# Kernel optimization log

Measured on AMD Instinct MI355X. Metric: run time of the kernel, lower is better.

Reference implementation:

```python
import jax, jax.numpy as jnp
import numpy as np

# dims: L=tgt len, S=src len, N=batch, E=embed, H=heads
L, S, N, E, H = 1024, 1024, 4, 1024, 16
HD = E // H  # head dim = 64


def setup_inputs() -> dict:
    key = jax.random.key(0)
    ks = jax.random.split(key, 7)
    w_scale = 0.02
    return {
        "query": jax.random.normal(ks[0], (L, N, E), jnp.float32),
        "key": jax.random.normal(ks[1], (S, N, E), jnp.float32),
        "value": jax.random.normal(ks[2], (S, N, E), jnp.float32),
        "in_proj_weight": jax.random.normal(ks[3], (3 * E, E), jnp.float32) * w_scale,
        "in_proj_bias": jax.random.normal(ks[4], (3 * E,), jnp.float32) * w_scale,
        "out_proj_weight": jax.random.normal(ks[5], (E, E), jnp.float32) * w_scale,
        "out_proj_bias": jax.random.normal(ks[6], (E,), jnp.float32) * w_scale,
    }


def reference(query, key, value, in_proj_weight, in_proj_bias,
              out_proj_weight, out_proj_bias):
    scaling = float(HD) ** -0.5
    # packed QKV projection, sliced exactly as the torch code does
    q = (query @ in_proj_weight[:E].T + in_proj_bias[:E]) * scaling        # (L,N,E)
    k = key @ in_proj_weight[E:2 * E].T + in_proj_bias[E:2 * E]            # (S,N,E)
    v = value @ in_proj_weight[2 * E:].T + in_proj_bias[2 * E:]            # (S,N,E)
    # split heads: (L,N,E) -> (N*H, L, HD)
    q = q.reshape(L, N * H, HD).transpose(1, 0, 2)
    k = k.reshape(S, N * H, HD).transpose(1, 0, 2)
    v = v.reshape(S, N * H, HD).transpose(1, 0, 2)
    scores = jnp.einsum('bld,bsd->bls', q, k)          # (N*H, L, S)
    attn = jax.nn.softmax(scores, axis=-1)
    sig = jax.nn.sigmoid(scores)                        # the need_sigmoid_weights variant
    out = jnp.einsum('bls,bsd->bld', attn, v)          # (N*H, L, HD)
    out = out.transpose(1, 0, 2).reshape(L, N, E)
    out = out @ out_proj_weight.T + out_proj_bias       # (L,N,E)
    # weights averaged over heads, as torch MHA returns: (N,L,S)
    attn_weights = attn.reshape(N, H, L, S).sum(axis=1) / H
    sig_weights = sig.reshape(N, H, L, S).sum(axis=1) / H
    return out, attn_weights, sig_weights
```

## Files before the change

kernel.cpp:

```cpp
#include <hip/hip_runtime.h>

#define L_DIM 1024
#define E_DIM 1024
#define NB 4
#define H_NUM 16
#define HD_DIM 64
#define T_TOK 4096
#define NHB 64

typedef float f32x4 __attribute__((ext_vector_type(4)));
typedef unsigned short u16x8 __attribute__((ext_vector_type(8)));
typedef unsigned short u16x4 __attribute__((ext_vector_type(4)));
typedef __bf16 bf16x8 __attribute__((ext_vector_type(8)));

__device__ inline unsigned short f2bf(float f) {
  unsigned int u = __builtin_bit_cast(unsigned int, f);
  u += 0x7FFFu + ((u >> 16) & 1u);
  return (unsigned short)(u >> 16);
}
__device__ inline f32x4 mfma16(u16x8 a, u16x8 b, f32x4 c) {
  return __builtin_amdgcn_mfma_f32_16x16x32_bf16(
      __builtin_bit_cast(bf16x8, a), __builtin_bit_cast(bf16x8, b), c, 0, 0, 0);
}

__device__ __forceinline__ void gl2lds16(const void* g, void* l) {
  auto gp = reinterpret_cast<const __attribute__((address_space(1))) unsigned int*>(
      reinterpret_cast<unsigned long long>(g));
  auto lp = reinterpret_cast<__attribute__((address_space(3))) unsigned int*>(
      static_cast<unsigned int>(reinterpret_cast<unsigned long long>(l)));
  __builtin_amdgcn_global_load_lds(gp, lp, 16, 0, 0);
}

__global__ __launch_bounds__(256) void cast_kernel(
    const float* __restrict__ s0, const float* __restrict__ s1,
    const float* __restrict__ s2, const float* __restrict__ s3,
    unsigned short* __restrict__ d0, unsigned short* __restrict__ d1,
    unsigned short* __restrict__ d2, unsigned short* __restrict__ d3,
    int n0, int n1, int n2, int n3) {
  const int y = blockIdx.y;
  const float* s = (y == 0) ? s0 : (y == 1) ? s1 : (y == 2) ? s2 : s3;
  unsigned short* d = (y == 0) ? d0 : (y == 1) ? d1 : (y == 2) ? d2 : d3;
  const int n = (y == 0) ? n0 : (y == 1) ? n1 : (y == 2) ? n2 : n3;
  int idx = (blockIdx.x * 256 + threadIdx.x) * 8;
  const int stride = gridDim.x * 256 * 8;
  for (; idx < n; idx += stride) {
    float4 a = *(const float4*)(s + idx);
    float4 b = *(const float4*)(s + idx + 4);
    u16x8 o = {f2bf(a.x), f2bf(a.y), f2bf(a.z), f2bf(a.w),
               f2bf(b.x), f2bf(b.y), f2bf(b.z), f2bf(b.w)};
    *(u16x8*)(d + idx) = o;
  }
}

__device__ __forceinline__ void stage_tile(const unsigned short* __restrict__ g,
                                           unsigned short* lbuf, int tid) {
  const int r = tid >> 2, c = tid & 3;
  const int sc = c ^ ((r ^ (r >> 2)) & 3);
  gl2lds16(g + (size_t)r * 1024 + sc * 8, lbuf + tid * 8);
  const int r2 = r + 64;
  gl2lds16(g + (size_t)r2 * 1024 + sc * 8, lbuf + (tid + 256) * 8);
}
__device__ __forceinline__ int frag_off(int r, int q) {
  return r * 32 + ((q ^ ((r ^ (r >> 2)) & 3)) << 3);
}

__global__ __launch_bounds__(256) void qkv_gemm(
    const unsigned short* __restrict__ qb, const unsigned short* __restrict__ kb,
    const unsigned short* __restrict__ vb, const unsigned short* __restrict__ Wb,
    const float* __restrict__ bias, unsigned short* __restrict__ q_hm,
    unsigned short* __restrict__ k_hm, unsigned short* __restrict__ v_t) {
  __shared__ __align__(16) unsigned short As[2][4096];
  __shared__ __align__(16) unsigned short Bs[2][4096];
  const int tid = threadIdx.x;
  const int bm = blockIdx.x, bn = blockIdx.y, z = blockIdx.z;
  const unsigned short* Ag = ((z == 0) ? qb : (z == 1) ? kb : vb) + (size_t)bm * 128 * 1024;
  const unsigned short* Bg = Wb + (size_t)z * 1048576 + (size_t)bn * 128 * 1024;
  const float* bc = bias + z * E_DIM;

  const int w = tid >> 6, lane = tid & 63;
  const int wm = w & 1, wn = w >> 1;
  const int quad = lane >> 4, l16 = lane & 15;

  f32x4 acc[4][4];
#pragma unroll
  for (int i = 0; i < 4; i++)
#pragma unroll
    for (int j = 0; j < 4; j++) { f32x4 zz = {0.f, 0.f, 0.f, 0.f}; acc[i][j] = zz; }

  stage_tile(Ag, As[0], tid);
  stage_tile(Bg, Bs[0], tid);

  for (int kk = 0; kk < 32; kk++) {
    __syncthreads();
    if (kk + 1 < 32) {
      const int bf = (kk + 1) & 1;
      stage_tile(Ag + (kk + 1) * 32, As[bf], tid);
      stage_tile(Bg + (kk + 1) * 32, Bs[bf], tid);
    }
    const int cb = kk & 1;
    u16x8 af[4], bfv[4];
#pragma unroll
    for (int mi = 0; mi < 4; mi++) {
      int r = wm * 64 + mi * 16 + l16;
      af[mi] = *(const u16x8*)&As[cb][frag_off(r, quad)];
    }
#pragma unroll
    for (int ni = 0; ni < 4; ni++) {
      int r = wn * 64 + ni * 16 + l16;
      bfv[ni] = *(const u16x8*)&Bs[cb][frag_off(r, quad)];
    }
#pragma unroll
    for (int mi = 0; mi < 4; mi++)
#pragma unroll
      for (int ni = 0; ni < 4; ni++)
        acc[mi][ni] = mfma16(af[mi], bfv[ni], acc[mi][ni]);
  }
#pragma unroll
  for (int ni = 0; ni < 4; ni++) {
    int col = bn * 128 + wn * 64 + ni * 16 + l16;
    float bv = bc[col];
    int h = col >> 6, d = col & 63;
#pragma unroll
    for (int mi = 0; mi < 4; mi++) {
#pragma unroll
      for (int r = 0; r < 4; r++) {
        int t = bm * 128 + wm * 64 + mi * 16 + quad * 4 + r;
        float v = acc[mi][ni][r] + bv;
        int nb = t & 3, pos = t >> 2;
        if (z == 0) {
          v *= 0.125f;
          q_hm[(size_t)((nb * 16 + h) * 1024 + pos) * 64 + d] = f2bf(v);
        } else if (z == 1) {
          k_hm[(size_t)((nb * 16 + h) * 1024 + pos) * 64 + d] = f2bf(v);
        } else {
          v_t[(size_t)((nb * 16 + h) * 64 + d) * 1024 + pos] = f2bf(v);
        }
      }
    }
  }
}

__global__ __launch_bounds__(256, 2) void attn_kernel(
    const unsigned short* __restrict__ q_hm, const unsigned short* __restrict__ k_hm,
    const unsigned short* __restrict__ v_t, unsigned short* __restrict__ o_h,
    float* __restrict__ m_ws, float* __restrict__ r_ws) {
  __shared__ __align__(16) unsigned short stage[8][4096];
  __shared__ __align__(16) unsigned short pt[2][32][68];
  __shared__ float red_m[4][32];
  __shared__ float red_s[4][32];

  const int tid = threadIdx.x;
  const int flat = blockIdx.x + (blockIdx.y << 5);
  const int nf = (flat & 7) * 256 + (flat >> 3);
  const int l0 = (nf & 31) * 32;
  const int b = nf >> 5;
  const int nb = b >> 4, h = b & 15;
  const int w = tid >> 6, lane = tid & 63;
  const int quad = lane >> 4, l16 = lane & 15;

  const int i1 = tid + 256;
  const int r0s = tid >> 3, c0s = tid & 7;
  const int r1s = i1 >> 3, c1s = i1 & 7;
  const int src0 = (c0s ^ (r0s & 7)) * 8;
  const int src1 = (c1s ^ (r1s & 7)) * 8;

  const unsigned short* kbase = k_hm + ((size_t)b << 16);
  const unsigned short* vbase = v_t + ((size_t)b << 16);

  u16x8 bq[2][2];
#pragma unroll
  for (int g = 0; g < 2; g++) {
    const unsigned short* qp =
        q_hm + ((size_t)(b * 1024 + l0 + g * 16 + l16) << 6) + quad * 8;
    bq[g][0] = *(const u16x8*)qp;
    bq[g][1] = *(const u16x8*)(qp + 32);
  }
  asm volatile("" ::: "memory");

  f32x4 acc[16][2];
#pragma unroll
  for (int j = 0; j < 16; j++)
#pragma unroll
    for (int g = 0; g < 2; g++) { f32x4 z = {0.f, 0.f, 0.f, 0.f}; acc[j][g] = z; }

#pragma unroll
  for (int t = 0; t < 3; t++) {
    gl2lds16(kbase + ((size_t)(t * 64 + r0s) << 6) + src0, &stage[t][tid * 8]);
    gl2lds16(kbase + ((size_t)(t * 64 + r1s) << 6) + src1, &stage[t][i1 * 8]);
  }

  const int myrow = w * 16 + l16;
  const int sw0 = ((quad ^ (l16 & 7)) * 8);
  const int sw1 = (((quad + 4) ^ (l16 & 7)) * 8);

#pragma unroll
  for (int j = 0; j < 16; j++) {
    if (j + 3 < 16) {
      gl2lds16(kbase + ((size_t)((j + 3) * 64 + r0s) << 6) + src0,
               &stage[(j + 3) & 7][tid * 8]);
      gl2lds16(kbase + ((size_t)((j + 3) * 64 + r1s) << 6) + src1,
               &stage[(j + 3) & 7][i1 * 8]);
    } else {
      const int vt = j + 3 - 16;
      gl2lds16(vbase + ((size_t)r0s << 10) + vt * 64 + src0,
               &stage[(j + 3) & 7][tid * 8]);
      gl2lds16(vbase + ((size_t)r1s << 10) + vt * 64 + src1,
               &stage[(j + 3) & 7][i1 * 8]);
    }
    asm volatile("s_waitcnt vmcnt(6)" ::: "memory");
    __builtin_amdgcn_s_barrier();
    asm volatile("" ::: "memory");
    const unsigned short* kt = &stage[j & 7][myrow * 64];
    u16x8 ak0 = *(const u16x8*)(kt + sw0);
    u16x8 ak1 = *(const u16x8*)(kt + sw1);
    acc[j][0] = mfma16(ak0, bq[0][0], acc[j][0]);
    acc[j][0] = mfma16(ak1, bq[0][1], acc[j][0]);
    acc[j][1] = mfma16(ak0, bq[1][0], acc[j][1]);
    acc[j][1] = mfma16(ak1, bq[1][1], acc[j][1]);
  }

  float lm0 = -3e38f, lm1 = -3e38f;
#pragma unroll
  for (int j = 0; j < 16; j++)
#pragma unroll
    for (int r = 0; r < 4; r++) {
      lm0 = fmaxf(lm0, acc[j][0][r]);
      lm1 = fmaxf(lm1, acc[j][1][r]);
    }
  lm0 = fmaxf(lm0, __shfl_xor(lm0, 16, 64));
  lm0 = fmaxf(lm0, __shfl_xor(lm0, 32, 64));
  lm1 = fmaxf(lm1, __shfl_xor(lm1, 16, 64));
  lm1 = fmaxf(lm1, __shfl_xor(lm1, 32, 64));
  if (lane < 16) { red_m[w][lane] = lm0; red_m[w][lane + 16] = lm1; }
  asm volatile("s_waitcnt lgkmcnt(0)" ::: "memory");
  __builtin_amdgcn_s_barrier();
  asm volatile("" ::: "memory");
  float m0 = fmaxf(fmaxf(red_m[0][l16], red_m[1][l16]),
                   fmaxf(red_m[2][l16], red_m[3][l16]));
  float m1 = fmaxf(fmaxf(red_m[0][l16 + 16], red_m[1][l16 + 16]),
                   fmaxf(red_m[2][l16 + 16], red_m[3][l16 + 16]));
  float mm = 0.f;
  if (tid < 32)
    mm = fmaxf(fmaxf(red_m[0][tid], red_m[1][tid]),
               fmaxf(red_m[2][tid], red_m[3][tid]));

  float ls0 = 0.f, ls1 = 0.f;
#pragma unroll
  for (int j = 0; j < 16; j++) {
#pragma unroll
    for (int r = 0; r < 4; r++) {
      float e0 = __expf(acc[j][0][r] - m0);
      float e1 = __expf(acc[j][1][r] - m1);
      acc[j][0][r] = e0;
      acc[j][1][r] = e1;
      ls0 += e0;
      ls1 += e1;
    }
  }
  ls0 += __shfl_xor(ls0, 16, 64);
  ls0 += __shfl_xor(ls0, 32, 64);
  ls1 += __shfl_xor(ls1, 16, 64);
  ls1 += __shfl_xor(ls1, 32, 64);
  if (lane < 16) { red_s[w][lane] = ls0; red_s[w][lane + 16] = ls1; }
  asm volatile("s_waitcnt lgkmcnt(0)" ::: "memory");
  __builtin_amdgcn_s_barrier();
  asm volatile("" ::: "memory");
  float rv0 = 1.0f / (red_s[0][l16] + red_s[1][l16] + red_s[2][l16] + red_s[3][l16]);
  float rv1 = 1.0f / (red_s[0][l16 + 16] + red_s[1][l16 + 16] +
                      red_s[2][l16 + 16] + red_s[3][l16 + 16]);
  float ssv = 1.f;
  if (tid < 32)
    ssv = red_s[0][tid] + red_s[1][tid] + red_s[2][tid] + red_s[3][tid];

  {
    u16x4 p0 = {f2bf(acc[0][0][0]), f2bf(acc[0][0][1]), f2bf(acc[0][0][2]), f2bf(acc[0][0][3])};
    u16x4 p1 = {f2bf(acc[0][1][0]), f2bf(acc[0][1][1]), f2bf(acc[0][1][2]), f2bf(acc[0][1][3])};
    *(u16x4*)&pt[0][l16][w * 16 + quad * 4] = p0;
    *(u16x4*)&pt[0][16 + l16][w * 16 + quad * 4] = p1;
  }

  f32x4 oacc0 = {0.f, 0.f, 0.f, 0.f};
  f32x4 oacc1 = {0.f, 0.f, 0.f, 0.f};
#pragma unroll
  for (int j = 0; j < 16; j++) {
    if (j < 13) {
      const int t = j + 3;
      gl2lds16(vbase + ((size_t)r0s << 10) + t * 64 + src0, &stage[t & 7][tid * 8]);
      gl2lds16(vbase + ((size_t)r1s << 10) + t * 64 + src1, &stage[t & 7][i1 * 8]);
      asm volatile("s_waitcnt vmcnt(6) lgkmcnt(0)" ::: "memory");
    } else if (j == 13) {
      asm volatile("s_waitcnt vmcnt(4) lgkmcnt(0)" ::: "memory");
    } else if (j == 14) {
      asm volatile("s_waitcnt vmcnt(2) lgkmcnt(0)" ::: "memory");
    } else {
      asm volatile("s_waitcnt vmcnt(0) lgkmcnt(0)" ::: "memory");
    }
    __builtin_amdgcn_s_barrier();
    asm volatile("" ::: "memory");
    if (j < 15) {
      const int bf = (j + 1) & 1;
      u16x4 p0 = {f2bf(acc[j + 1][0][0]), f2bf(acc[j + 1][0][1]),
                  f2bf(acc[j + 1][0][2]), f2bf(acc[j + 1][0][3])};
      u16x4 p1 = {f2bf(acc[j + 1][1][0]), f2bf(acc[j + 1][1][1]),
                  f2bf(acc[j + 1][1][2]), f2bf(acc[j + 1][1][3])};
      *(u16x4*)&pt[bf][l16][w * 16 + quad * 4] = p0;
      *(u16x4*)&pt[bf][16 + l16][w * 16 + quad * 4] = p1;
    }
    const unsigned short* vt = &stage[j & 7][myrow * 64];
    u16x8 bv0 = *(const u16x8*)(vt + sw0);
    u16x8 bv1 = *(const u16x8*)(vt + sw1);
    u16x8 ap00 = *(const u16x8*)&pt[j & 1][l16][quad * 8];
    u16x8 ap01 = *(const u16x8*)&pt[j & 1][l16][32 + quad * 8];
    u16x8 ap10 = *(const u16x8*)&pt[j & 1][16 + l16][quad * 8];
    u16x8 ap11 = *(const u16x8*)&pt[j & 1][16 + l16][32 + quad * 8];
    oacc0 = mfma16(ap00, bv0, oacc0);
    oacc0 = mfma16(ap01, bv1, oacc0);
    oacc1 = mfma16(ap10, bv0, oacc1);
    oacc1 = mfma16(ap11, bv1, oacc1);
  }

  if (tid < 32) {
    m_ws[b * 1024 + l0 + tid] = mm;
    r_ws[b * 1024 + l0 + tid] = 1.0f / ssv;
  }

#pragma unroll
  for (int r = 0; r < 4; r++) {
    int lr = quad * 4 + r;
    float rr0 = __shfl(rv0, lr, 64);
    float rr1 = __shfl(rv1, lr, 64);
    int t0 = (l0 + lr) * 4 + nb;
    int t1 = (l0 + 16 + lr) * 4 + nb;
    o_h[((size_t)t0 << 10) + h * 64 + w * 16 + l16] = f2bf(oacc0[r] * rr0);
    o_h[((size_t)t1 << 10) + h * 64 + w * 16 + l16] = f2bf(oacc1[r] * rr1);
  }
}

__global__ __launch_bounds__(256, 2) void weights_kernel(
    const unsigned short* __restrict__ q_hm, const unsigned short* __restrict__ k_hm,
    const float* __restrict__ m_ws, const float* __restrict__ r_ws,
    float* __restrict__ attn_out, float* __restrict__ sig_out) {
  __shared__ __align__(16) unsigned short qs[4][4096];
  __shared__ __align__(16) unsigned short ks[4][4096];
  __shared__ float ml[16][64];
  __shared__ float rl[16][64];
  __shared__ float cl[16][64];

  const int tid = threadIdx.x;
  const int flat = blockIdx.x + (blockIdx.y << 4) + (blockIdx.z << 8);
  const int xcd = flat & 7, local = flat >> 3;
  const int nb = xcd >> 1;
  const int idx2 = ((xcd & 1) << 7) + local;
  const int l0 = (idx2 >> 4) << 6;
  const int s0 = (idx2 & 15) << 6;

  const int w = tid >> 6, lane = tid & 63;
  const int quad = lane >> 4, l16 = lane & 15;

  const int i1 = tid + 256;
  const int r0s = tid >> 3, c0s = tid & 7;
  const int r1s = i1 >> 3, c1s = i1 & 7;
  const int src0 = (c0s ^ (r0s & 7)) * 8;
  const int src1 = (c1s ^ (r1s & 7)) * 8;

  {
    int idx = tid * 4;
    int hh = idx >> 6, ii = idx & 63;
    int bb = nb * 16 + hh;
    float4 mv4 = *(const float4*)&m_ws[bb * 1024 + l0 + ii];
    float4 rv4 = *(const float4*)&r_ws[bb * 1024 + l0 + ii];
    *(float4*)&ml[hh][ii] = mv4;
    *(float4*)&rl[hh][ii] = rv4;
    float4 cv4 = {__expf(-mv4.x), __expf(-mv4.y), __expf(-mv4.z), __expf(-mv4.w)};
    *(float4*)&cl[hh][ii] = cv4;
  }

  const int sw0 = ((quad ^ (l16 & 7)) * 8);
  const int sw1 = (((quad + 4) ^ (l16 & 7)) * 8);

  auto stageQK = [&](int h) {
    const int bb = nb * 16 + h;
    const unsigned short* qb = q_hm + ((size_t)(bb * 1024 + l0) << 6);
    const unsigned short* kb = k_hm + ((size_t)(bb * 1024 + s0) << 6);
    const int bf = h & 3;
    gl2lds16(qb + (r0s << 6) + src0, &qs[bf][tid * 8]);
    gl2lds16(qb + (r1s << 6) + src1, &qs[bf][i1 * 8]);
    gl2lds16(kb + (r0s << 6) + src0, &ks[bf][tid * 8]);
    gl2lds16(kb + (r1s << 6) + src1, &ks[bf][i1 * 8]);
  };

  f32x4 accA[4], accS[4];
#pragma unroll
  for (int i = 0; i < 4; i++) {
    f32x4 zz = {0.f, 0.f, 0.f, 0.f};
    accA[i] = zz; accS[i] = zz;
  }

  stageQK(0);
  stageQK(1);
  asm volatile("s_waitcnt lgkmcnt(0)" ::: "memory");

  auto computeH = [&](int h) {
    const int bf = h & 3;
    const unsigned short* qt = &qs[bf][(w * 16 + l16) * 64];
    u16x8 a0 = *(const u16x8*)(qt + sw0);
    u16x8 a1 = *(const u16x8*)(qt + sw1);
    f32x4 mv = *(const f32x4*)&ml[h][w * 16 + quad * 4];
    f32x4 rv = *(const f32x4*)&rl[h][w * 16 + quad * 4];
    f32x4 cv = *(const f32x4*)&cl[h][w * 16 + quad * 4];
#pragma unroll
    for (int ni = 0; ni < 4; ni++) {
      const unsigned short* kt = &ks[bf][(ni * 16 + l16) * 64];
      u16x8 b0 = *(const u16x8*)(kt + sw0);
      u16x8 b1 = *(const u16x8*)(kt + sw1);
      f32x4 scv = {0.f, 0.f, 0.f, 0.f};
      scv = mfma16(a0, b0, scv);
      scv = mfma16(a1, b1, scv);
#pragma unroll
      for (int r = 0; r < 4; r++) {
        float e = __expf(scv[r] - mv[r]);
        accA[ni][r] += e * rv[r];
        accS[ni][r] += e * __builtin_amdgcn_rcpf(e + cv[r]);
      }
    }
  };

#pragma unroll 1
  for (int h = 0; h < 14; ++h) {
    stageQK(h + 2);
    asm volatile("s_waitcnt vmcnt(8)" ::: "memory");
    __builtin_amdgcn_s_barrier();
    asm volatile("" ::: "memory");
    computeH(h);
  }
  asm volatile("s_waitcnt vmcnt(4)" ::: "memory");
  __builtin_amdgcn_s_barrier();
  asm volatile("" ::: "memory");
  computeH(14);
  asm volatile("s_waitcnt vmcnt(0)" ::: "memory");
  __builtin_amdgcn_s_barrier();
  asm volatile("" ::: "memory");
  computeH(15);

  const float inv_h = 1.0f / 16.0f;
  const int lrow0 = l0 + w * 16;
#pragma unroll
  for (int ni = 0; ni < 4; ni++) {
#pragma unroll
    for (int r = 0; r < 4; r++) {
      int l = lrow0 + quad * 4 + r;
      int s = s0 + ni * 16 + l16;
      size_t idx = ((size_t)nb * 1024 + l) * 1024 + s;
      attn_out[idx] = accA[ni][r] * inv_h;
      sig_out[idx] = accS[ni][r] * inv_h;
    }
  }
}

__global__ __launch_bounds__(256) void out_gemm(
    const unsigned short* __restrict__ o_h, const unsigned short* __restrict__ Wb,
    const float* __restrict__ bias, float* __restrict__ out) {
  __shared__ __align__(16) unsigned short As[2][4096];
  __shared__ __align__(16) unsigned short Bs[2][4096];
  const int tid = threadIdx.x;
  const int bm = blockIdx.x, bn = blockIdx.y;
  const unsigned short* Ag = o_h + (size_t)bm * 128 * 1024;
  const unsigned short* Bg = Wb + (size_t)bn * 128 * 1024;

  const int w = tid >> 6, lane = tid & 63;
  const int wm = w & 1, wn = w >> 1;
  const int quad = lane >> 4, l16 = lane & 15;

  f32x4 acc[4][4];
#pragma unroll
  for (int i = 0; i < 4; i++)
#pragma unroll
    for (int j = 0; j < 4; j++) { f32x4 zz = {0.f, 0.f, 0.f, 0.f}; acc[i][j] = zz; }

  stage_tile(Ag, As[0], tid);
  stage_tile(Bg, Bs[0], tid);

  for (int kk = 0; kk < 32; kk++) {
    __syncthreads();
    if (kk + 1 < 32) {
      const int bf = (kk + 1) & 1;
      stage_tile(Ag + (kk + 1) * 32, As[bf], tid);
      stage_tile(Bg + (kk + 1) * 32, Bs[bf], tid);
    }
    const int cb = kk & 1;
    u16x8 af[4], bfv[4];
#pragma unroll
    for (int mi = 0; mi < 4; mi++) {
      int r = wm * 64 + mi * 16 + l16;
      af[mi] = *(const u16x8*)&As[cb][frag_off(r, quad)];
    }
#pragma unroll
    for (int ni = 0; ni < 4; ni++) {
      int r = wn * 64 + ni * 16 + l16;
      bfv[ni] = *(const u16x8*)&Bs[cb][frag_off(r, quad)];
    }
#pragma unroll
    for (int mi = 0; mi < 4; mi++)
#pragma unroll
      for (int ni = 0; ni < 4; ni++)
        acc[mi][ni] = mfma16(af[mi], bfv[ni], acc[mi][ni]);
  }
#pragma unroll
  for (int ni = 0; ni < 4; ni++) {
    int col = bn * 128 + wn * 64 + ni * 16 + l16;
    float bv = bias[col];
#pragma unroll
    for (int mi = 0; mi < 4; mi++) {
#pragma unroll
      for (int r = 0; r < 4; r++) {
        int t = bm * 128 + wm * 64 + mi * 16 + quad * 4 + r;
        out[(size_t)t * E_DIM + col] = acc[mi][ni][r] + bv;
      }
    }
  }
}

extern "C" void kernel_launch(void* const* d_in, const int* in_sizes, int n_in,
                              void* d_out, int out_size, void* d_ws, size_t ws_size,
                              hipStream_t stream) {
  const float* qin  = (const float*)d_in[0];
  const float* kin  = (const float*)d_in[1];
  const float* vin  = (const float*)d_in[2];
  const float* Wqkv = (const float*)d_in[3];
  const float* bqkv = (const float*)d_in[4];
  const float* Wout = (const float*)d_in[5];
  const float* bout = (const float*)d_in[6];
  float* out      = (float*)d_out;
  float* attn_out = out + 4194304;
  float* sig_out  = out + 8388608;

  unsigned short* q_hm = (unsigned short*)d_ws;
  unsigned short* k_hm = q_hm + 4194304;
  unsigned short* v_t  = q_hm + 8388608;
  unsigned short* o_h  = q_hm + 12582912;
  float* m_ws = (float*)(q_hm + 16777216);
  float* r_ws = m_ws + 65536;

  unsigned short* qb = (unsigned short*)(out + 4194304);
  unsigned short* kb = qb + 4194304;
  unsigned short* vb = qb + 8388608;
  unsigned short* Wqkvb = o_h;
  unsigned short* Woutb = v_t;

  cast_kernel<<<dim3(2048, 4), 256, 0, stream>>>(
      qin, kin, vin, Wqkv, qb, kb, vb, Wqkvb,
      4194304, 4194304, 4194304, 3145728);
  qkv_gemm<<<dim3(32, 8, 3), 256, 0, stream>>>(qb, kb, vb, Wqkvb, bqkv,
                                               q_hm, k_hm, v_t);
  attn_kernel<<<dim3(32, 64), 256, 0, stream>>>(q_hm, k_hm, v_t, o_h, m_ws, r_ws);
  cast_kernel<<<dim3(512, 1), 256, 0, stream>>>(
      Wout, Wout, Wout, Wout, Woutb, Woutb, Woutb, Woutb,
      1048576, 0, 0, 0);
  weights_kernel<<<dim3(16, 16, 4), 256, 0, stream>>>(q_hm, k_hm, m_ws, r_ws,
                                                      attn_out, sig_out);
  out_gemm<<<dim3(32, 8), 256, 0, stream>>>(o_h, Woutb, bout, out);
}
```

Measured before the change: 252.2 us.

## Deepen GEMM LDS pipeline to five stages and swizzle block order

New measurement: 266.4 us. 5.6% more time.

```diff
diff --git a/kernel.cpp b/kernel.cpp
--- a/kernel.cpp
+++ b/kernel.cpp
@@ -69,10 +69,12 @@
     const unsigned short* __restrict__ vb, const unsigned short* __restrict__ Wb,
     const float* __restrict__ bias, unsigned short* __restrict__ q_hm,
     unsigned short* __restrict__ k_hm, unsigned short* __restrict__ v_t) {
-  __shared__ __align__(16) unsigned short As[2][4096];
-  __shared__ __align__(16) unsigned short Bs[2][4096];
+  __shared__ __align__(16) unsigned short As[5][4096];
+  __shared__ __align__(16) unsigned short Bs[5][4096];
   const int tid = threadIdx.x;
-  const int bm = blockIdx.x, bn = blockIdx.y, z = blockIdx.z;
+  const int flat = blockIdx.x + (blockIdx.y << 5) + (blockIdx.z << 8);
+  const int nf = (flat & 7) * 96 + (flat >> 3);
+  const int bm = nf & 31, bn = (nf >> 5) & 7, z = nf >> 8;
   const unsigned short* Ag = ((z == 0) ? qb : (z == 1) ? kb : vb) + (size_t)bm * 128 * 1024;
   const unsigned short* Bg = Wb + (size_t)z * 1048576 + (size_t)bn * 128 * 1024;
   const float* bc = bias + z * E_DIM;
@@ -87,17 +89,29 @@
 #pragma unroll
     for (int j = 0; j < 4; j++) { f32x4 zz = {0.f, 0.f, 0.f, 0.f}; acc[i][j] = zz; }
 
-  stage_tile(Ag, As[0], tid);
-  stage_tile(Bg, Bs[0], tid);
-
+#pragma unroll
+  for (int t = 0; t < 3; t++) {
+    stage_tile(Ag + t * 32, As[t], tid);
+    stage_tile(Bg + t * 32, Bs[t], tid);
+  }
+
+  int cb = 0, sb = 3;
+#pragma unroll 1
   for (int kk = 0; kk < 32; kk++) {
-    __syncthreads();
-    if (kk + 1 < 32) {
-      const int bf = (kk + 1) & 1;
-      stage_tile(Ag + (kk + 1) * 32, As[bf], tid);
-      stage_tile(Bg + (kk + 1) * 32, Bs[bf], tid);
-    }
-    const int cb = kk & 1;
+    if (kk < 29) {
+      stage_tile(Ag + (kk + 3) * 32, As[sb], tid);
+      stage_tile(Bg + (kk + 3) * 32, Bs[sb], tid);
+      sb = (sb == 4) ? 0 : sb + 1;
+      asm volatile("s_waitcnt vmcnt(12)" ::: "memory");
+    } else if (kk == 29) {
+      asm volatile("s_waitcnt vmcnt(8)" ::: "memory");
+    } else if (kk == 30) {
+      asm volatile("s_waitcnt vmcnt(4)" ::: "memory");
+    } else {
+      asm volatile("s_waitcnt vmcnt(0)" ::: "memory");
+    }
+    __builtin_amdgcn_s_barrier();
+    asm volatile("" ::: "memory");
     u16x8 af[4], bfv[4];
 #pragma unroll
     for (int mi = 0; mi < 4; mi++) {
@@ -114,6 +128,7 @@
 #pragma unroll
       for (int ni = 0; ni < 4; ni++)
         acc[mi][ni] = mfma16(af[mi], bfv[ni], acc[mi][ni]);
+    cb = (cb == 4) ? 0 : cb + 1;
   }
 #pragma unroll
   for (int ni = 0; ni < 4; ni++) {
@@ -460,10 +475,12 @@
 __global__ __launch_bounds__(256) void out_gemm(
     const unsigned short* __restrict__ o_h, const unsigned short* __restrict__ Wb,
     const float* __restrict__ bias, float* __restrict__ out) {
-  __shared__ __align__(16) unsigned short As[2][4096];
-  __shared__ __align__(16) unsigned short Bs[2][4096];
+  __shared__ __align__(16) unsigned short As[5][4096];
+  __shared__ __align__(16) unsigned short Bs[5][4096];
   const int tid = threadIdx.x;
-  const int bm = blockIdx.x, bn = blockIdx.y;
+  const int flat = blockIdx.x + (blockIdx.y << 5);
+  const int nf = (flat & 7) * 32 + (flat >> 3);
+  const int bm = nf & 31, bn = nf >> 5;
   const unsigned short* Ag = o_h + (size_t)bm * 128 * 1024;
   const unsigned short* Bg = Wb + (size_t)bn * 128 * 1024;
 
@@ -477,17 +494,29 @@
 #pragma unroll
     for (int j = 0; j < 4; j++) { f32x4 zz = {0.f, 0.f, 0.f, 0.f}; acc[i][j] = zz; }
 
-  stage_tile(Ag, As[0], tid);
-  stage_tile(Bg, Bs[0], tid);
-
+#pragma unroll
+  for (int t = 0; t < 3; t++) {
+    stage_tile(Ag + t * 32, As[t], tid);
+    stage_tile(Bg + t * 32, Bs[t], tid);
+  }
+
+  int cb = 0, sb = 3;
+#pragma unroll 1
   for (int kk = 0; kk < 32; kk++) {
-    __syncthreads();
-    if (kk + 1 < 32) {
-      const int bf = (kk + 1) & 1;
-      stage_tile(Ag + (kk + 1) * 32, As[bf], tid);
-      stage_tile(Bg + (kk + 1) * 32, Bs[bf], tid);
-    }
-    const int cb = kk & 1;
+    if (kk < 29) {
+      stage_tile(Ag + (kk + 3) * 32, As[sb], tid);
+      stage_tile(Bg + (kk + 3) * 32, Bs[sb], tid);
+      sb = (sb == 4) ? 0 : sb + 1;
+      asm volatile("s_waitcnt vmcnt(12)" ::: "memory");
+    } else if (kk == 29) {
+      asm volatile("s_waitcnt vmcnt(8)" ::: "memory");
+    } else if (kk == 30) {
+      asm volatile("s_waitcnt vmcnt(4)" ::: "memory");
+    } else {
+      asm volatile("s_waitcnt vmcnt(0)" ::: "memory");
+    }
+    __builtin_amdgcn_s_barrier();
+    asm volatile("" ::: "memory");
     u16x8 af[4], bfv[4];
 #pragma unroll
     for (int mi = 0; mi < 4; mi++) {
@@ -504,6 +533,7 @@
 #pragma unroll
       for (int ni = 0; ni < 4; ni++)
         acc[mi][ni] = mfma16(af[mi], bfv[ni], acc[mi][ni]);
+    cb = (cb == 4) ? 0 : cb + 1;
   }
 #pragma unroll
   for (int ni = 0; ni < 4; ni++) {
```
